# Kernel tuning notes

Hardware: AMD Instinct MI355X
Metric: run time of the kernel (lower is better)

The kernel has to match this reference:

```python
import jax, jax.numpy as jnp
import numpy as np

B, L, D, KSIZE = 8, 2048, 768, 8


def setup_inputs() -> dict:
    key = jax.random.key(0)
    k1, k2, k3, k4, k5 = jax.random.split(key, 5)
    s = 1.0 / np.sqrt(D)  # torch default GRU init scale
    x = jax.random.normal(k1, (B, L, D), dtype=jnp.float32)
    w_ih = jax.random.uniform(k2, (D, 3 * D), jnp.float32, -s, s)
    w_hh = jax.random.uniform(k3, (D, 3 * D), jnp.float32, -s, s)
    b_ih = jax.random.uniform(k4, (3 * D,), jnp.float32, -s, s)
    b_hh = jax.random.uniform(k5, (3 * D,), jnp.float32, -s, s)
    return {"x": x, "w_ih": w_ih, "w_hh": w_hh, "b_ih": b_ih, "b_hh": b_hh, "ksize": KSIZE}


def reference(x, w_ih, w_hh, b_ih, b_hh, ksize):
    """LocalRNN forward: sliding window of size ksize (zero left-pad), GRU over
    each window, return last hidden state per position -> [B, L, D].
    Instead of materializing the redundant [B*L, ksize, D] windowed tensor,
    we run the ksize-step recurrence over all positions in parallel: the j-th
    GRU step for window ending at t consumes xpad[:, t + j, :].
    """
    Bb, Ll, Dd = x.shape
    xpad = jnp.concatenate([jnp.zeros((Bb, ksize - 1, Dd), x.dtype), x], axis=1)
    # precompute input-side gate activations once: [B, L+k-1, 3D]
    gx_all = xpad @ w_ih + b_ih

    def step(h, j):
        gx = jax.lax.dynamic_slice_in_dim(gx_all, j, Ll, axis=1)  # [B, L, 3D]
        gh = h @ w_hh + b_hh                                       # [B, L, 3D]
        xr, xz, xn = jnp.split(gx, 3, axis=-1)
        hr, hz, hn = jnp.split(gh, 3, axis=-1)
        r = jax.nn.sigmoid(xr + hr)
        z = jax.nn.sigmoid(xz + hz)
        n = jnp.tanh(xn + r * hn)
        h_new = (1.0 - z) * n + z * h
        return h_new, None

    h0 = jnp.zeros((Bb, Ll, Dd), x.dtype)
    h, _ = jax.lax.scan(step, h0, jnp.arange(ksize))
    return h
```

## Files before the change

### kernel.cpp

```cpp
#include <hip/hip_runtime.h>
#include <stdint.h>
#include <stddef.h>

using short8 = __attribute__((ext_vector_type(8))) short;
using f32x4  = __attribute__((ext_vector_type(4))) float;

#define BB 8
#define LL 2048
#define DD 768
#define KS 8
#define ND 2304
#define NT 12
#define NBN_GX 18
#define NBD_GRU 12

__device__ __forceinline__ float bf2f(unsigned short u) {
  union { uint32_t i; float f; } v; v.i = ((uint32_t)u) << 16; return v.f;
}
__device__ __forceinline__ unsigned short f2bf(float f) {
  union { float f; uint32_t i; } v; v.f = f;
  return (unsigned short)((v.i + 0x7FFFu + ((v.i >> 16) & 1u)) >> 16);
}
__device__ __forceinline__ float sigm(float x) { return 1.0f / (1.0f + __expf(-x)); }
__device__ __forceinline__ float tanh_fast(float x) {
  return 2.0f / (1.0f + __expf(-2.0f * x)) - 1.0f;
}
__device__ __forceinline__ void gload_lds16(const void* g, void* lds) {
  __builtin_amdgcn_global_load_lds(
      (const __attribute__((address_space(1))) void*)g,
      (__attribute__((address_space(3))) void*)lds, 16, 0, 0);
}

__device__ __forceinline__ void swz_blocks(int bid, int nbm, int nbn,
                                           int* mb, int* nb) {
  int gsz = 8 * nbn;
  int g = bid / gsz;
  int rem = bid - g * gsz;
  int gg = nbm - g * 8; if (gg > 8) gg = 8;
  *nb = rem / gg;
  *mb = g * 8 + (rem - *nb * gg);
}

__global__ void detect_k(const uint32_t* __restrict__ x, int* __restrict__ flag) {
  int t = threadIdx.x;
  uint32_t w = x[t * 16];
  int e = (int)((w >> 7) & 0xFF);
  int isbf = (e >= 112 && e <= 136) ? 1 : 0;
  unsigned long long m = __ballot(isbf);
  if (t == 0) *flag = (__popcll(m) >= 32) ? 1 : 0;
}

__global__ void transpose_k(const void* __restrict__ in,
                            unsigned short* __restrict__ out, int R, int C,
                            const int* __restrict__ flagp) {
  const bool bf = (*flagp != 0);
  __shared__ unsigned short t[32][33];
  int c0 = blockIdx.x * 32, r0 = blockIdx.y * 32;
  int tx = threadIdx.x, ty = threadIdx.y;
#pragma unroll
  for (int i = ty; i < 32; i += 8) {
    size_t idx = (size_t)(r0 + i) * C + c0 + tx;
    t[i][tx] = bf ? ((const unsigned short*)in)[idx]
                  : f2bf(((const float*)in)[idx]);
  }
  __syncthreads();
#pragma unroll
  for (int i = ty; i < 32; i += 8)
    out[(size_t)(c0 + i) * R + r0 + tx] = t[tx][i];
}

__global__ void conv_bias(const void* __restrict__ in,
                          unsigned short* __restrict__ out, int n,
                          const int* __restrict__ flagp) {
  const bool bf = (*flagp != 0);
  int i = blockIdx.x * 256 + threadIdx.x;
  if (i >= n) return;
  out[i] = bf ? ((const unsigned short*)in)[i] : f2bf(((const float*)in)[i]);
}

__global__ void conv_x(const void* __restrict__ xv,
                       unsigned short* __restrict__ xpadc,
                       int Uc, int t0, int total8,
                       const int* __restrict__ flagp) {
  const bool bf = (*flagp != 0);
  int idx = blockIdx.x * 256 + threadIdx.x;
  if (idx >= total8) return;
  size_t e = (size_t)idx * 8;
  int d = (int)(e % DD);
  size_t ru = e / DD;
  int u = (int)(ru % Uc);
  int b = (int)(ru / Uc);
  int p = t0 + u;
  short8 v = {0, 0, 0, 0, 0, 0, 0, 0};
  if (p >= KS - 1) {
    size_t base = ((size_t)b * LL + (p - (KS - 1))) * DD + d;
    if (bf) {
      v = *(const short8*)((const unsigned short*)xv + base);
    } else {
      const float* fp = (const float*)xv + base;
      float4 a = *(const float4*)fp, b4 = *(const float4*)(fp + 4);
      v[0] = (short)f2bf(a.x); v[1] = (short)f2bf(a.y);
      v[2] = (short)f2bf(a.z); v[3] = (short)f2bf(a.w);
      v[4] = (short)f2bf(b4.x); v[5] = (short)f2bf(b4.y);
      v[6] = (short)f2bf(b4.z); v[7] = (short)f2bf(b4.w);
    }
  }
  *(short8*)&xpadc[e] = v;
}

__global__ __launch_bounds__(256, 3) void gemm_gx(
    const unsigned short* __restrict__ A, const unsigned short* __restrict__ WT,
    const unsigned short* __restrict__ bias, unsigned short* __restrict__ Cout,
    int Mrows, int nbm) {
  __shared__ __align__(16) unsigned short Al[128 * 64];
  __shared__ __align__(16) unsigned short Bl[128 * 64];
  const int tid = threadIdx.x, lane = tid & 63, wv = tid >> 6;
  const int wm = wv >> 1, wn = wv & 1;
  int mb, nb; swz_blocks(blockIdx.x, nbm, NBN_GX, &mb, &nb);
  const int m0 = mb * 128, n0 = nb * 128;
  const int h16 = lane >> 4, l16 = lane & 15;

  const unsigned short* asrc[4];
  const unsigned short* bsrc[4];
#pragma unroll
  for (int it = 0; it < 4; ++it) {
    int c = it * 256 + tid;
    int row = c >> 3;
    int slotg = (c & 7) ^ (row & 7);
    int grow = m0 + row; if (grow >= Mrows) grow = Mrows - 1;
    asrc[it] = A + (size_t)grow * DD + slotg * 8;
    bsrc[it] = WT + (size_t)(n0 + row) * DD + slotg * 8;
  }
  char* aldst = (char*)Al + (wv * 1024);
  char* bldst = (char*)Bl + (wv * 1024);

  f32x4 acc[4][4] = {};

  for (int kt = 0; kt < NT; ++kt) {
    const int ko = kt * 64;
#pragma unroll
    for (int it = 0; it < 4; ++it)
      gload_lds16(asrc[it] + ko, aldst + it * 4096);
#pragma unroll
    for (int it = 0; it < 4; ++it)
      gload_lds16(bsrc[it] + ko, bldst + it * 4096);
    __syncthreads();
#pragma unroll
    for (int s = 0; s < 2; ++s) {
      short8 af[4], bfr[4];
#pragma unroll
      for (int i = 0; i < 4; ++i) {
        int row = wm * 64 + i * 16 + l16;
        af[i] = *(const short8*)&Al[row * 64 + (((s * 4 + h16) ^ (row & 7)) * 8)];
      }
#pragma unroll
      for (int jn = 0; jn < 4; ++jn) {
        int row = wn * 64 + jn * 16 + l16;
        bfr[jn] = *(const short8*)&Bl[row * 64 + (((s * 4 + h16) ^ (row & 7)) * 8)];
      }
#pragma unroll
      for (int i = 0; i < 4; ++i)
#pragma unroll
        for (int jn = 0; jn < 4; ++jn)
          acc[i][jn] = __builtin_amdgcn_mfma_f32_16x16x32_bf16(af[i], bfr[jn], acc[i][jn], 0, 0, 0);
    }
    if (kt + 1 < NT) __syncthreads();
  }

#pragma unroll
  for (int jn = 0; jn < 4; ++jn) {
    int n = n0 + wn * 64 + jn * 16 + l16;
    float bv = bf2f(bias[n]);
#pragma unroll
    for (int i = 0; i < 4; ++i) {
      int mb2 = m0 + wm * 64 + i * 16 + 4 * h16;
#pragma unroll
      for (int r = 0; r < 4; ++r) {
        int m = mb2 + r;
        if (m < Mrows) Cout[(size_t)m * ND + n] = f2bf(acc[i][jn][r] + bv);
      }
    }
  }
}

__global__ void gru_step0(const unsigned short* __restrict__ gx, int Uc,
                          const unsigned short* __restrict__ bhh,
                          unsigned short* __restrict__ hout, int lgTc) {
  int idx = blockIdx.x * 256 + threadIdx.x;
  int d0 = (idx % (DD / 8)) * 8;
  int row = idx / (DD / 8);
  int b = row >> lgTc, t = row & ((1 << lgTc) - 1);
  size_t gxrow = ((size_t)b * Uc + t) * ND;
  short8 vr = *(const short8*)(gx + gxrow + d0);
  short8 vz = *(const short8*)(gx + gxrow + DD + d0);
  short8 vn = *(const short8*)(gx + gxrow + 2 * DD + d0);
  short8 br = *(const short8*)(bhh + d0);
  short8 bz = *(const short8*)(bhh + DD + d0);
  short8 bn = *(const short8*)(bhh + 2 * DD + d0);
  short8 o;
#pragma unroll
  for (int k = 0; k < 8; ++k) {
    float r = sigm(bf2f((unsigned short)vr[k]) + bf2f((unsigned short)br[k]));
    float z = sigm(bf2f((unsigned short)vz[k]) + bf2f((unsigned short)bz[k]));
    float n = tanh_fast(bf2f((unsigned short)vn[k]) + r * bf2f((unsigned short)bn[k]));
    o[k] = (short)f2bf((1.0f - z) * n);
  }
  *(short8*)(hout + (size_t)row * DD + d0) = o;
}

__global__ __launch_bounds__(256, 3) void gemm_gru_step(
    const unsigned short* __restrict__ Hc, const unsigned short* __restrict__ WT,
    const unsigned short* __restrict__ bhh, const unsigned short* __restrict__ gx,
    int Uc, void* __restrict__ Hn, int hnBS, int hnOff, int j, int lgTc,
    const int* __restrict__ flagp, int isFinal, int nbm) {
  __shared__ __align__(16) unsigned short Al[128 * 64];
  __shared__ __align__(16) unsigned short Bl[192 * 64];
  const bool bfm = (*flagp != 0);
  const int tid = threadIdx.x, lane = tid & 63, wv = tid >> 6;
  const int wm = wv >> 1, wd = wv & 1;
  int mb, db; swz_blocks(blockIdx.x, nbm, NBD_GRU, &mb, &db);
  const int m0 = mb * 128, d0 = db * 64;
  const int h16 = lane >> 4, l16 = lane & 15;
  const int tmask = (1 << lgTc) - 1;

  const int r0i = tid >> 3;
  const int slotg = (tid & 7) ^ (r0i & 7);
  const unsigned short* abase = Hc + (size_t)(m0 + r0i) * DD + slotg * 8;
  const unsigned short* bbase = WT + (size_t)(d0 + r0i) * DD + slotg * 8;
  char* aldst = (char*)Al + (wv * 1024);
  char* bldst = (char*)Bl + (wv * 1024);

  f32x4 acc[4][2][3] = {};

  for (int kt = 0; kt < NT; ++kt) {
    const int ko = kt * 64;
#pragma unroll
    for (int it = 0; it < 4; ++it)
      gload_lds16(abase + (size_t)it * (32 * DD) + ko, aldst + it * 4096);
#pragma unroll
    for (int it = 0; it < 6; ++it) {
      const size_t boff = (size_t)(it >> 1) * (DD * DD) + (size_t)(it & 1) * (32 * DD);
      gload_lds16(bbase + boff + ko, bldst + it * 4096);
    }
    __syncthreads();
#pragma unroll
    for (int s = 0; s < 2; ++s) {
      short8 af[4];
#pragma unroll
      for (int i = 0; i < 4; ++i) {
        int row = wm * 64 + i * 16 + l16;
        af[i] = *(const short8*)&Al[row * 64 + (((s * 4 + h16) ^ (row & 7)) * 8)];
      }
      short8 bfr[2][3];
#pragma unroll
      for (int jd = 0; jd < 2; ++jd)
#pragma unroll
        for (int g = 0; g < 3; ++g) {
          int row = g * 64 + wd * 32 + jd * 16 + l16;
          bfr[jd][g] = *(const short8*)&Bl[row * 64 + (((s * 4 + h16) ^ (row & 7)) * 8)];
        }
#pragma unroll
      for (int i = 0; i < 4; ++i)
#pragma unroll
        for (int jd = 0; jd < 2; ++jd)
#pragma unroll
          for (int g = 0; g < 3; ++g)
            acc[i][jd][g] = __builtin_amdgcn_mfma_f32_16x16x32_bf16(af[i], bfr[jd][g], acc[i][jd][g], 0, 0, 0);
    }
    if (kt + 1 < NT) __syncthreads();
  }

#pragma unroll
  for (int jd = 0; jd < 2; ++jd) {
    int d = d0 + wd * 32 + jd * 16 + l16;
    float br = bf2f(bhh[d]), bz = bf2f(bhh[DD + d]), bn = bf2f(bhh[2 * DD + d]);
#pragma unroll
    for (int i = 0; i < 4; ++i) {
      int mbase = m0 + wm * 64 + i * 16 + 4 * h16;
#pragma unroll
      for (int r2 = 0; r2 < 4; ++r2) {
        int m = mbase + r2;
        int b = m >> lgTc, t = m & tmask;
        size_t gxrow = ((size_t)b * Uc + t + j) * ND;
        float xr = bf2f(gx[gxrow + d]);
        float xz = bf2f(gx[gxrow + DD + d]);
        float xn = bf2f(gx[gxrow + 2 * DD + d]);
        float gr = acc[i][jd][0][r2] + br;
        float gz = acc[i][jd][1][r2] + bz;
        float gn = acc[i][jd][2][r2] + bn;
        float rr = sigm(xr + gr);
        float zz = sigm(xz + gz);
        float nn = tanh_fast(xn + rr * gn);
        float ho = bf2f(Hc[(size_t)m * DD + d]);
        float val = (1.0f - zz) * nn + zz * ho;
        size_t hnrow = (size_t)b * hnBS + hnOff + t;
        if (isFinal && !bfm) ((float*)Hn)[hnrow * DD + d] = val;
        else ((unsigned short*)Hn)[hnrow * DD + d] = f2bf(val);
      }
    }
  }
}

extern "C" void kernel_launch(void* const* d_in, const int* in_sizes, int n_in,
                              void* d_out, int out_size, void* d_ws, size_t ws_size,
                              hipStream_t stream) {
  const void* x    = d_in[0];
  const void* w_ih = d_in[1];
  const void* w_hh = d_in[2];
  const void* b_ih = d_in[3];
  const void* b_hh = d_in[4];

  const size_t wTbytes = (size_t)ND * DD * 2;
  const size_t hdr = 2 * wTbytes + 2 * 4608 + 4096;

  int Tc = 64;
  for (int tc = 2048; tc >= 64; tc >>= 1) {
    size_t hBsz  = (size_t)BB * tc * DD * 2;
    size_t xpsz  = (size_t)BB * (tc + KS - 1) * DD * 2;
    size_t uni   = hBsz > xpsz ? hBsz : xpsz;
    size_t need = hdr +
                  (size_t)BB * (tc + KS - 1) * ND * 2 +
                  (size_t)BB * tc * DD * 2 +
                  uni;
    if (need <= ws_size) { Tc = tc; break; }
  }
  int lgTc = 0; while ((1 << lgTc) < Tc) ++lgTc;
  const int Uc = Tc + KS - 1;
  const int Mc = BB * Tc;
  const int Mg = BB * Uc;

  char* ws = (char*)d_ws;
  unsigned short* wihT = (unsigned short*)ws; ws += wTbytes;
  unsigned short* whhT = (unsigned short*)ws; ws += wTbytes;
  unsigned short* bihB = (unsigned short*)ws; ws += 4608;
  unsigned short* bhhB = (unsigned short*)ws; ws += 4608;
  int* flag            = (int*)ws;            ws += 4096;
  unsigned short* gxc  = (unsigned short*)ws; ws += (size_t)Mg * ND * 2;
  unsigned short* hA   = (unsigned short*)ws; ws += (size_t)Mc * DD * 2;
  unsigned short* hB   = (unsigned short*)ws;
  unsigned short* xpadc = hB;

  detect_k<<<1, 64, 0, stream>>>((const uint32_t*)x, flag);
  transpose_k<<<dim3(ND / 32, DD / 32), dim3(32, 8), 0, stream>>>(w_ih, wihT, DD, ND, flag);
  transpose_k<<<dim3(ND / 32, DD / 32), dim3(32, 8), 0, stream>>>(w_hh, whhT, DD, ND, flag);
  conv_bias<<<(ND + 255) / 256, 256, 0, stream>>>(b_ih, bihB, ND, flag);
  conv_bias<<<(ND + 255) / 256, 256, 0, stream>>>(b_hh, bhhB, ND, flag);

  const int nbmGx = (Mg + 127) / 128;
  const int nbmGru = Mc / 128;

  for (int t0 = 0; t0 < LL; t0 += Tc) {
    int total8 = Mg * (DD / 8);
    conv_x<<<(total8 + 255) / 256, 256, 0, stream>>>(x, xpadc, Uc, t0, total8, flag);

    gemm_gx<<<nbmGx * NBN_GX, 256, 0, stream>>>(
        xpadc, wihT, bihB, gxc, Mg, nbmGx);

    gru_step0<<<(Mc * (DD / 8)) / 256, 256, 0, stream>>>(gxc, Uc, bhhB, hA, lgTc);

    unsigned short* cur = hA;
    for (int j = 1; j <= 7; ++j) {
      int isFinal = (j == 7);
      void* dst = isFinal ? d_out : (void*)((cur == hA) ? hB : hA);
      int hnBS = isFinal ? LL : Tc;
      int hnOff = isFinal ? t0 : 0;
      gemm_gru_step<<<nbmGru * NBD_GRU, 256, 0, stream>>>(
          cur, whhT, bhhB, gxc, Uc, dst, hnBS, hnOff, j, lgTc, flag, isFinal, nbmGru);
      if (!isFinal) cur = (cur == hA) ? hB : hA;
    }
  }
}
```

Before: 702.5 us.

## Fuse GRU step-0 into input GEMM and interleave gate activations per channel

The input-projection GEMM now tiles by hidden channel with all three gates per block, so its epilogue can compute the first GRU step directly and write h0, which removes the separate gru_step0 kernel and its reread of gx. Gate pre-activations are stored interleaved as r,z,n plus a zero pad per channel (8 bytes), so each recurrent step's epilogue does one 8-byte load instead of three scattered 2-byte loads. The padding raises gx storage and write traffic by a third, which may shrink the chunk size chosen for the workspace.

```diff
diff --git a/kernel.cpp b/kernel.cpp
--- a/kernel.cpp
+++ b/kernel.cpp
@@ -3,6 +3,7 @@
 #include <stddef.h>
 
 using short8 = __attribute__((ext_vector_type(8))) short;
+using short4v = __attribute__((ext_vector_type(4))) short;
 using f32x4  = __attribute__((ext_vector_type(4))) float;
 
 #define BB 8
@@ -11,8 +12,7 @@
 #define KS 8
 #define ND 2304
 #define NT 12
-#define NBN_GX 18
-#define NBD_GRU 12
+#define NBD 12
 
 __device__ __forceinline__ float bf2f(unsigned short u) {
   union { uint32_t i; float f; } v; v.i = ((uint32_t)u) << 16; return v.f;
@@ -110,31 +110,30 @@
 
 __global__ __launch_bounds__(256, 3) void gemm_gx(
     const unsigned short* __restrict__ A, const unsigned short* __restrict__ WT,
-    const unsigned short* __restrict__ bias, unsigned short* __restrict__ Cout,
-    int Mrows, int nbm) {
+    const unsigned short* __restrict__ bih, const unsigned short* __restrict__ bhh,
+    unsigned short* __restrict__ gxp, unsigned short* __restrict__ h0,
+    int Mrows, int Uc, int Tcc, int nbm) {
   __shared__ __align__(16) unsigned short Al[128 * 64];
-  __shared__ __align__(16) unsigned short Bl[128 * 64];
+  __shared__ __align__(16) unsigned short Bl[192 * 64];
   const int tid = threadIdx.x, lane = tid & 63, wv = tid >> 6;
-  const int wm = wv >> 1, wn = wv & 1;
-  int mb, nb; swz_blocks(blockIdx.x, nbm, NBN_GX, &mb, &nb);
-  const int m0 = mb * 128, n0 = nb * 128;
+  const int wm = wv >> 1, wd = wv & 1;
+  int mb, db; swz_blocks(blockIdx.x, nbm, NBD, &mb, &db);
+  const int m0 = mb * 128, d0 = db * 64;
   const int h16 = lane >> 4, l16 = lane & 15;
 
+  const int r0i = tid >> 3;
+  const int slotg = (tid & 7) ^ (r0i & 7);
   const unsigned short* asrc[4];
-  const unsigned short* bsrc[4];
 #pragma unroll
   for (int it = 0; it < 4; ++it) {
-    int c = it * 256 + tid;
-    int row = c >> 3;
-    int slotg = (c & 7) ^ (row & 7);
-    int grow = m0 + row; if (grow >= Mrows) grow = Mrows - 1;
+    int grow = m0 + it * 32 + r0i; if (grow >= Mrows) grow = Mrows - 1;
     asrc[it] = A + (size_t)grow * DD + slotg * 8;
-    bsrc[it] = WT + (size_t)(n0 + row) * DD + slotg * 8;
-  }
+  }
+  const unsigned short* bbase = WT + (size_t)(d0 + r0i) * DD + slotg * 8;
   char* aldst = (char*)Al + (wv * 1024);
   char* bldst = (char*)Bl + (wv * 1024);
 
-  f32x4 acc[4][4] = {};
+  f32x4 acc[4][2][3] = {};
 
   for (int kt = 0; kt < NT; ++kt) {
     const int ko = kt * 64;
@@ -142,75 +141,72 @@
     for (int it = 0; it < 4; ++it)
       gload_lds16(asrc[it] + ko, aldst + it * 4096);
 #pragma unroll
-    for (int it = 0; it < 4; ++it)
-      gload_lds16(bsrc[it] + ko, bldst + it * 4096);
+    for (int it = 0; it < 6; ++it) {
+      const size_t boff = (size_t)(it >> 1) * (DD * DD) + (size_t)(it & 1) * (32 * DD);
+      gload_lds16(bbase + boff + ko, bldst + it * 4096);
+    }
     __syncthreads();
 #pragma unroll
     for (int s = 0; s < 2; ++s) {
-      short8 af[4], bfr[4];
+      short8 af[4];
 #pragma unroll
       for (int i = 0; i < 4; ++i) {
         int row = wm * 64 + i * 16 + l16;
         af[i] = *(const short8*)&Al[row * 64 + (((s * 4 + h16) ^ (row & 7)) * 8)];
       }
-#pragma unroll
-      for (int jn = 0; jn < 4; ++jn) {
-        int row = wn * 64 + jn * 16 + l16;
-        bfr[jn] = *(const short8*)&Bl[row * 64 + (((s * 4 + h16) ^ (row & 7)) * 8)];
+      short8 bfr[2][3];
+#pragma unroll
+      for (int jd = 0; jd < 2; ++jd)
+#pragma unroll
+        for (int g = 0; g < 3; ++g) {
+          int row = g * 64 + wd * 32 + jd * 16 + l16;
+          bfr[jd][g] = *(const short8*)&Bl[row * 64 + (((s * 4 + h16) ^ (row & 7)) * 8)];
+        }
+#pragma unroll
+      for (int i = 0; i < 4; ++i)
+#pragma unroll
+        for (int jd = 0; jd < 2; ++jd)
+#pragma unroll
+          for (int g = 0; g < 3; ++g)
+            acc[i][jd][g] = __builtin_amdgcn_mfma_f32_16x16x32_bf16(af[i], bfr[jd][g], acc[i][jd][g], 0, 0, 0);
+    }
+    if (kt + 1 < NT) __syncthreads();
+  }
+
+#pragma unroll
+  for (int jd = 0; jd < 2; ++jd) {
+    int d = d0 + wd * 32 + jd * 16 + l16;
+    float bir = bf2f(bih[d]), biz = bf2f(bih[DD + d]), bin_ = bf2f(bih[2 * DD + d]);
+    float bhr = bf2f(bhh[d]), bhz = bf2f(bhh[DD + d]), bhn = bf2f(bhh[2 * DD + d]);
+#pragma unroll
+    for (int i = 0; i < 4; ++i) {
+      int mbase = m0 + wm * 64 + i * 16 + 4 * h16;
+#pragma unroll
+      for (int r2 = 0; r2 < 4; ++r2) {
+        int m = mbase + r2;
+        if (m >= Mrows) continue;
+        float gr = acc[i][jd][0][r2] + bir;
+        float gz = acc[i][jd][1][r2] + biz;
+        float gn = acc[i][jd][2][r2] + bin_;
+        short4v pk;
+        pk[0] = (short)f2bf(gr); pk[1] = (short)f2bf(gz);
+        pk[2] = (short)f2bf(gn); pk[3] = 0;
+        *(short4v*)(gxp + (size_t)m * (DD * 4) + d * 4) = pk;
+        int b = m / Uc, u = m - b * Uc;
+        if (u < Tcc) {
+          float r = sigm(gr + bhr);
+          float z = sigm(gz + bhz);
+          float n = tanh_fast(gn + r * bhn);
+          h0[((size_t)b * Tcc + u) * DD + d] = f2bf((1.0f - z) * n);
+        }
       }
-#pragma unroll
-      for (int i = 0; i < 4; ++i)
-#pragma unroll
-        for (int jn = 0; jn < 4; ++jn)
-          acc[i][jn] = __builtin_amdgcn_mfma_f32_16x16x32_bf16(af[i], bfr[jn], acc[i][jn], 0, 0, 0);
-    }
-    if (kt + 1 < NT) __syncthreads();
-  }
-
-#pragma unroll
-  for (int jn = 0; jn < 4; ++jn) {
-    int n = n0 + wn * 64 + jn * 16 + l16;
-    float bv = bf2f(bias[n]);
-#pragma unroll
-    for (int i = 0; i < 4; ++i) {
-      int mb2 = m0 + wm * 64 + i * 16 + 4 * h16;
-#pragma unroll
-      for (int r = 0; r < 4; ++r) {
-        int m = mb2 + r;
-        if (m < Mrows) Cout[(size_t)m * ND + n] = f2bf(acc[i][jn][r] + bv);
-      }
-    }
-  }
-}
-
-__global__ void gru_step0(const unsigned short* __restrict__ gx, int Uc,
-                          const unsigned short* __restrict__ bhh,
-                          unsigned short* __restrict__ hout, int lgTc) {
-  int idx = blockIdx.x * 256 + threadIdx.x;
-  int d0 = (idx % (DD / 8)) * 8;
-  int row = idx / (DD / 8);
-  int b = row >> lgTc, t = row & ((1 << lgTc) - 1);
-  size_t gxrow = ((size_t)b * Uc + t) * ND;
-  short8 vr = *(const short8*)(gx + gxrow + d0);
-  short8 vz = *(const short8*)(gx + gxrow + DD + d0);
-  short8 vn = *(const short8*)(gx + gxrow + 2 * DD + d0);
-  short8 br = *(const short8*)(bhh + d0);
-  short8 bz = *(const short8*)(bhh + DD + d0);
-  short8 bn = *(const short8*)(bhh + 2 * DD + d0);
-  short8 o;
-#pragma unroll
-  for (int k = 0; k < 8; ++k) {
-    float r = sigm(bf2f((unsigned short)vr[k]) + bf2f((unsigned short)br[k]));
-    float z = sigm(bf2f((unsigned short)vz[k]) + bf2f((unsigned short)bz[k]));
-    float n = tanh_fast(bf2f((unsigned short)vn[k]) + r * bf2f((unsigned short)bn[k]));
-    o[k] = (short)f2bf((1.0f - z) * n);
-  }
-  *(short8*)(hout + (size_t)row * DD + d0) = o;
+    }
+  }
 }
 
 __global__ __launch_bounds__(256, 3) void gemm_gru_step(
     const unsigned short* __restrict__ Hc, const unsigned short* __restrict__ WT,
-    const unsigned short* __restrict__ bhh, const unsigned short* __restrict__ gx,
+    const unsigned short* __restrict__ bhh, const unsigned short* __restrict__ gxp,
     int Uc, void* __restrict__ Hn, int hnBS, int hnOff, int j, int lgTc,
     const int* __restrict__ flagp, int isFinal, int nbm) {
   __shared__ __align__(16) unsigned short Al[128 * 64];
@@ -218,7 +214,7 @@
   const bool bfm = (*flagp != 0);
   const int tid = threadIdx.x, lane = tid & 63, wv = tid >> 6;
   const int wm = wv >> 1, wd = wv & 1;
-  int mb, db; swz_blocks(blockIdx.x, nbm, NBD_GRU, &mb, &db);
+  int mb, db; swz_blocks(blockIdx.x, nbm, NBD, &mb, &db);
   const int m0 = mb * 128, d0 = db * 64;
   const int h16 = lane >> 4, l16 = lane & 15;
   const int tmask = (1 << lgTc) - 1;
@@ -281,10 +277,11 @@
       for (int r2 = 0; r2 < 4; ++r2) {
         int m = mbase + r2;
         int b = m >> lgTc, t = m & tmask;
-        size_t gxrow = ((size_t)b * Uc + t + j) * ND;
-        float xr = bf2f(gx[gxrow + d]);
-        float xz = bf2f(gx[gxrow + DD + d]);
-        float xn = bf2f(gx[gxrow + 2 * DD + d]);
+        size_t gxrow = (size_t)b * Uc + t + j;
+        short4v pk = *(const short4v*)(gxp + gxrow * (DD * 4) + d * 4);
+        float xr = bf2f((unsigned short)pk[0]);
+        float xz = bf2f((unsigned short)pk[1]);
+        float xn = bf2f((unsigned short)pk[2]);
         float gr = acc[i][jd][0][r2] + br;
         float gz = acc[i][jd][1][r2] + bz;
         float gn = acc[i][jd][2][r2] + bn;
@@ -319,7 +316,7 @@
     size_t xpsz  = (size_t)BB * (tc + KS - 1) * DD * 2;
     size_t uni   = hBsz > xpsz ? hBsz : xpsz;
     size_t need = hdr +
-                  (size_t)BB * (tc + KS - 1) * ND * 2 +
+                  (size_t)BB * (tc + KS - 1) * DD * 8 +
                   (size_t)BB * tc * DD * 2 +
                   uni;
     if (need <= ws_size) { Tc = tc; break; }
@@ -335,7 +332,7 @@
   unsigned short* bihB = (unsigned short*)ws; ws += 4608;
   unsigned short* bhhB = (unsigned short*)ws; ws += 4608;
   int* flag            = (int*)ws;            ws += 4096;
-  unsigned short* gxc  = (unsigned short*)ws; ws += (size_t)Mg * ND * 2;
+  unsigned short* gxc  = (unsigned short*)ws; ws += (size_t)Mg * DD * 8;
   unsigned short* hA   = (unsigned short*)ws; ws += (size_t)Mc * DD * 2;
   unsigned short* hB   = (unsigned short*)ws;
   unsigned short* xpadc = hB;
@@ -353,10 +350,8 @@
     int total8 = Mg * (DD / 8);
     conv_x<<<(total8 + 255) / 256, 256, 0, stream>>>(x, xpadc, Uc, t0, total8, flag);
 
-    gemm_gx<<<nbmGx * NBN_GX, 256, 0, stream>>>(
-        xpadc, wihT, bihB, gxc, Mg, nbmGx);
-
-    gru_step0<<<(Mc * (DD / 8)) / 256, 256, 0, stream>>>(gxc, Uc, bhhB, hA, lgTc);
+    gemm_gx<<<nbmGx * NBD, 256, 0, stream>>>(
+        xpadc, wihT, bihB, bhhB, gxc, hA, Mg, Uc, Tc, nbmGx);
 
     unsigned short* cur = hA;
     for (int j = 1; j <= 7; ++j) {
@@ -364,7 +359,7 @@
       void* dst = isFinal ? d_out : (void*)((cur == hA) ? hB : hA);
       int hnBS = isFinal ? LL : Tc;
       int hnOff = isFinal ? t0 : 0;
-      gemm_gru_step<<<nbmGru * NBD_GRU, 256, 0, stream>>>(
+      gemm_gru_step<<<nbmGru * NBD, 256, 0, stream>>>(
           cur, whhT, bhhB, gxc, Uc, dst, hnBS, hnOff, j, lgTc, flag, isFinal, nbmGru);
       if (!isFinal) cur = (cur == hA) ? hB : hA;
     }
```

After: 696.7 us. Within noise of the previous version (-0.8%).
